# Optimization experiments

Measured on AMD Instinct MI355X. Metric: run time of the kernel, lower is better.

The kernel has to match this reference:

```python
import jax, jax.numpy as jnp
import numpy as np

BN_EPS = 1e-5

# Octonion multiplication table: hamilton block (r, c) = SIGN[c][r] * a[IDX[c][r]]
IDX = np.array([
    [0,1,2,3,4,5,6,7],
    [1,0,3,2,5,4,7,6],
    [2,3,0,1,6,7,4,5],
    [3,2,1,0,7,6,5,4],
    [4,5,6,7,0,1,2,3],
    [5,4,7,6,1,0,3,2],
    [6,7,4,5,2,3,0,1],
    [7,6,5,4,3,2,1,0]], dtype=np.int32)
SIGN = np.array([
    [ 1, 1, 1, 1, 1, 1, 1, 1],
    [ 1,-1, 1,-1, 1,-1,-1, 1],
    [ 1,-1,-1, 1, 1, 1,-1,-1],
    [ 1, 1,-1,-1, 1,-1, 1,-1],
    [ 1,-1,-1,-1,-1, 1, 1, 1],
    [ 1, 1,-1, 1,-1,-1,-1, 1],
    [ 1, 1, 1,-1,-1, 1,-1,-1],
    [ 1,-1, 1, 1,-1,-1, 1,-1]], dtype=np.float32)

def make_octonion_mul(kernel):
    # kernel: [in/8, out]; split cols into 8 chunks a0..a7 of [in/8, out/8]
    in8, out = kernel.shape
    out8 = out // 8
    a = kernel.reshape(in8, 8, out8).transpose(1, 0, 2)  # [8, in/8, out/8]
    blocks = jnp.asarray(SIGN)[:, :, None, None] * a[jnp.asarray(IDX)]  # [c, r, in/8, out/8]
    # hamilton[r*in8:(r+1)*in8, c*out8:(c+1)*out8] = blocks[c, r]
    return jnp.transpose(blocks, (1, 2, 0, 3)).reshape(8 * in8, out)  # [in, out]

def setup_inputs() -> dict:
    key = jax.random.key(0)
    ks = jax.random.split(key, 5)
    N, E, D_IN, D_OUT = 100000, 3200000, 256, 256
    stdv = float(np.sqrt(6.0 / (D_IN // 8 + D_OUT)))
    return {
        "x": jax.random.normal(ks[0], (N, D_IN), dtype=jnp.float32),
        "weight": jax.random.uniform(ks[1], (D_IN // 8, D_OUT), dtype=jnp.float32,
                                      minval=-stdv, maxval=stdv),
        "gamma": jnp.ones((D_OUT,), dtype=jnp.float32),
        "beta": jnp.zeros((D_OUT,), dtype=jnp.float32),
        "edge_weight": jax.random.uniform(ks[2], (E,), dtype=jnp.float32),
        "edge_src": jax.random.randint(ks[3], (E,), 0, N, dtype=jnp.int32),
        "edge_dst": jax.random.randint(ks[4], (E,), 0, N, dtype=jnp.int32),
    }

def reference(x, weight, gamma, beta, edge_weight, edge_src, edge_dst):
    N = x.shape[0]
    hamilton = make_octonion_mul(weight)          # [in, out]
    support = x @ hamilton                        # [N, out]
    # sparse adjacency aggregation: out[dst] += w * support[src]
    msgs = edge_weight[:, None] * support[edge_src]
    out = jax.ops.segment_sum(msgs, edge_dst, num_segments=N)  # [N, out]
    # BatchNorm1d (training mode: batch stats, biased variance)
    mean = jnp.mean(out, axis=0)
    var = jnp.var(out, axis=0)
    out = (out - mean) * jax.lax.rsqrt(var + BN_EPS) * gamma + beta
    return jnp.tanh(out)
```

## Files before the change

### kernel.cpp

```cpp
#include <hip/hip_runtime.h>
#include <cmath>

#define NB 512
#define CHUNK 8192

typedef short short8 __attribute__((ext_vector_type(8)));
typedef float f32x4 __attribute__((ext_vector_type(4)));

__constant__ int c_IDX[64] = {
  0,1,2,3,4,5,6,7,
  1,0,3,2,5,4,7,6,
  2,3,0,1,6,7,4,5,
  3,2,1,0,7,6,5,4,
  4,5,6,7,0,1,2,3,
  5,4,7,6,1,0,3,2,
  6,7,4,5,2,3,0,1,
  7,6,5,4,3,2,1,0};
__constant__ float c_SIGN[64] = {
  1,1,1,1,1,1,1,1,
  1,-1,1,-1,1,-1,-1,1,
  1,-1,-1,1,1,1,-1,-1,
  1,1,-1,-1,1,-1,1,-1,
  1,-1,-1,-1,-1,1,1,1,
  1,1,-1,1,-1,-1,-1,1,
  1,1,1,-1,-1,1,-1,-1,
  1,-1,1,1,-1,-1,1,-1};

__device__ inline unsigned bf16_rne(float f) {
  unsigned u = __float_as_uint(f);
  return (u + 0x7fffu + ((u >> 16) & 1u)) >> 16;
}
__device__ inline unsigned bfpack(float lo, float hi) {
  return bf16_rne(lo) | (bf16_rne(hi) << 16);
}

__global__ __launch_bounds__(256) void hamT_kernel(const float* __restrict__ weight,
                                                   unsigned short* __restrict__ hi,
                                                   unsigned short* __restrict__ lo) {
  int idx = blockIdx.x * 256 + threadIdx.x;
  int col = idx >> 8, k = idx & 255;
  int r = k >> 5, i = k & 31, c = col >> 5, o = col & 31;
  float v = c_SIGN[c * 8 + r] * weight[i * 256 + c_IDX[c * 8 + r] * 32 + o];
  unsigned hb = bf16_rne(v);
  float hf = __uint_as_float(hb << 16);
  hi[idx] = (unsigned short)hb;
  lo[idx] = (unsigned short)bf16_rne(v - hf);
}

__global__ __launch_bounds__(256) void cvt_kernel(const float4* __restrict__ x4,
                                                  uint2* __restrict__ xh, size_t n4) {
  size_t idx = (size_t)blockIdx.x * 256 + threadIdx.x;
  size_t stride = (size_t)gridDim.x * 256;
  for (size_t i = idx; i < n4; i += stride) {
    float4 v = x4[i];
    xh[i] = make_uint2(bfpack(v.x, v.y), bfpack(v.z, v.w));
  }
}

__global__ __launch_bounds__(256) void binhist_kernel(const int* __restrict__ dst,
                                                      int* __restrict__ binTot,
                                                      int E, int N) {
  __shared__ int h[NB];
  int tid = threadIdx.x;
  for (int i = tid; i < NB; i += 256) h[i] = 0;
  __syncthreads();
  int base = blockIdx.x * CHUNK;
  int end = base + CHUNK; if (end > E) end = E;
  for (int i = base + tid; i < end; i += 256)
    atomicAdd(&h[(int)((long long)dst[i] * NB / N)], 1);
  __syncthreads();
  for (int i = tid; i < NB; i += 256)
    if (h[i]) atomicAdd(&binTot[i], h[i]);
}

__global__ __launch_bounds__(512) void binscan_kernel(const int* __restrict__ binTot,
                                                      int* __restrict__ binStart,
                                                      int* __restrict__ binCursor, int E) {
  __shared__ int wsum[8], wbase[8];
  int tid = threadIdx.x, lane = tid & 63, wid = tid >> 6;
  int v = binTot[tid];
  int incl = v;
  #pragma unroll
  for (int d = 1; d < 64; d <<= 1) { int u = __shfl_up(incl, d); if (lane >= d) incl += u; }
  if (lane == 63) wsum[wid] = incl;
  __syncthreads();
  if (tid == 0) { int s = 0; for (int w = 0; w < 8; w++) { wbase[w] = s; s += wsum[w]; } }
  __syncthreads();
  int excl = wbase[wid] + incl - v;
  binStart[tid] = excl;
  binCursor[tid] = excl;
  if (tid == NB - 1) binStart[NB] = E;
}

__global__ __launch_bounds__(256) void bin_scatter(const int* __restrict__ src,
                                                   const int* __restrict__ dst,
                                                   const float* __restrict__ w,
                                                   int* __restrict__ binCursor,
                                                   int2* __restrict__ bb, int E, int N) {
  __shared__ int hist[NB];
  __shared__ int lcur[NB];
  int tid = threadIdx.x;
  int base = blockIdx.x * CHUNK;
  int end = base + CHUNK; if (end > E) end = E;
  for (int i = tid; i < NB; i += 256) hist[i] = 0;
  __syncthreads();
  for (int i = base + tid; i < end; i += 256)
    atomicAdd(&hist[(int)((long long)dst[i] * NB / N)], 1);
  __syncthreads();
  for (int i = tid; i < NB; i += 256) {
    int h = hist[i];
    lcur[i] = h ? atomicAdd(&binCursor[i], h) : 0;
  }
  __syncthreads();
  for (int i = base + tid; i < end; i += 256) {
    int d = dst[i];
    int b = (int)((long long)d * NB / N);
    int d0 = (int)(((long long)b * N + NB - 1) / NB);
    int pos = atomicAdd(&lcur[b], 1);
    bb[pos] = make_int2(src[i] | ((d - d0) << 24), __float_as_int(w[i]));
  }
}

__global__ __launch_bounds__(256) void bin_place(const int2* __restrict__ bb,
                                                 const int* __restrict__ binStart,
                                                 int* __restrict__ off,
                                                 int* __restrict__ cnt,
                                                 int2* __restrict__ edges, int N) {
  __shared__ int lcnt[208];
  __shared__ int loff[208];
  int b = blockIdx.x, tid = threadIdx.x;
  int d0 = (int)(((long long)b * N + NB - 1) / NB);
  int d1 = (int)(((long long)(b + 1) * N + NB - 1) / NB);
  if (d1 > N) d1 = N;
  int nd = d1 - d0;
  int e0 = binStart[b], e1 = binStart[b + 1];
  for (int i = tid; i < nd; i += 256) lcnt[i] = 0;
  __syncthreads();
  for (int i = e0 + tid; i < e1; i += 256)
    atomicAdd(&lcnt[((unsigned)bb[i].x) >> 24], 1);
  __syncthreads();
  if (tid == 0) {
    int s = e0;
    for (int i = 0; i < nd; i++) { loff[i] = s; s += lcnt[i]; }
  }
  __syncthreads();
  for (int i = tid; i < nd; i += 256) {
    off[d0 + i] = loff[i];
    cnt[d0 + i] = lcnt[i];
  }
  __syncthreads();
  for (int i = tid; i < nd; i += 256) lcnt[i] = loff[i];
  __syncthreads();
  for (int i = e0 + tid; i < e1; i += 256) {
    int2 e = bb[i];
    int pos = atomicAdd(&lcnt[((unsigned)e.x) >> 24], 1);
    edges[pos] = make_int2(e.x & 0xFFFFFF, e.y);
  }
}

__device__ inline void acc4(float& a0, float& a1, float& a2, float& a3,
                            uint2 v, float w) {
  a0 = fmaf(w, __uint_as_float(v.x << 16), a0);
  a1 = fmaf(w, __uint_as_float(v.x & 0xffff0000u), a1);
  a2 = fmaf(w, __uint_as_float(v.y << 16), a2);
  a3 = fmaf(w, __uint_as_float(v.y & 0xffff0000u), a3);
}

__global__ __launch_bounds__(256) void gather_kernel(const uint2* __restrict__ x8,
                                                     const int2* __restrict__ edges,
                                                     const int* __restrict__ off,
                                                     const int* __restrict__ cnt,
                                                     uint2* __restrict__ agg8, int N) {
  int d = blockIdx.x * 4 + (threadIdx.x >> 6);
  if (d >= N) return;
  int c = threadIdx.x & 63;
  int start = off[d], n = cnt[d];
  float a0 = 0.f, a1 = 0.f, a2 = 0.f, a3 = 0.f;
  int t = 0;
  for (; t + 8 <= n; t += 8) {
    int2 e0 = edges[start + t + 0];
    int2 e1 = edges[start + t + 1];
    int2 e2 = edges[start + t + 2];
    int2 e3 = edges[start + t + 3];
    int2 e4 = edges[start + t + 4];
    int2 e5 = edges[start + t + 5];
    int2 e6 = edges[start + t + 6];
    int2 e7 = edges[start + t + 7];
    uint2 v0 = x8[(size_t)e0.x * 64 + c];
    uint2 v1 = x8[(size_t)e1.x * 64 + c];
    uint2 v2 = x8[(size_t)e2.x * 64 + c];
    uint2 v3 = x8[(size_t)e3.x * 64 + c];
    uint2 v4 = x8[(size_t)e4.x * 64 + c];
    uint2 v5 = x8[(size_t)e5.x * 64 + c];
    uint2 v6 = x8[(size_t)e6.x * 64 + c];
    uint2 v7 = x8[(size_t)e7.x * 64 + c];
    acc4(a0, a1, a2, a3, v0, __int_as_float(e0.y));
    acc4(a0, a1, a2, a3, v1, __int_as_float(e1.y));
    acc4(a0, a1, a2, a3, v2, __int_as_float(e2.y));
    acc4(a0, a1, a2, a3, v3, __int_as_float(e3.y));
    acc4(a0, a1, a2, a3, v4, __int_as_float(e4.y));
    acc4(a0, a1, a2, a3, v5, __int_as_float(e5.y));
    acc4(a0, a1, a2, a3, v6, __int_as_float(e6.y));
    acc4(a0, a1, a2, a3, v7, __int_as_float(e7.y));
  }
  for (; t < n; t++) {
    int2 e0 = edges[start + t];
    uint2 v0 = x8[(size_t)e0.x * 64 + c];
    acc4(a0, a1, a2, a3, v0, __int_as_float(e0.y));
  }
  agg8[(size_t)d * 64 + c] = make_uint2(bfpack(a0, a1), bfpack(a2, a3));
}

__global__ __launch_bounds__(512) void mfma_gemm(const uint4* __restrict__ aggh,
                                                 const unsigned short* __restrict__ hamT_hi,
                                                 const unsigned short* __restrict__ hamT_lo,
                                                 float* __restrict__ bnsum,
                                                 float* __restrict__ out, int N) {
  __shared__ __align__(16) unsigned short Al[128 * 256];
  __shared__ float csum[256], csq[256];
  const int tid = threadIdx.x;
  const int row0 = blockIdx.x * 128;
  const int lane = tid & 63, wv = tid >> 6;
  const int wm = wv >> 2, wn = wv & 3;

  if (tid < 256) { csum[tid] = 0.f; csq[tid] = 0.f; }

  #pragma unroll
  for (int it = 0; it < 8; it++) {
    int cidx = it * 512 + tid;
    int row = cidx >> 5, c16 = cidx & 31;
    int rg = row0 + row;
    uint4 v = make_uint4(0u, 0u, 0u, 0u);
    if (rg < N) v = aggh[(size_t)rg * 32 + c16];
    *(uint4*)((char*)Al + row * 512 + ((c16 * 16) ^ ((row & 7) << 4))) = v;
  }
  __syncthreads();

  f32x4 acc[4][4];
  #pragma unroll
  for (int m = 0; m < 4; m++)
    #pragma unroll
    for (int n = 0; n < 4; n++) acc[m][n] = (f32x4)0.f;

  const char* bh = (const char*)hamT_hi;
  const char* bl = (const char*)hamT_lo;
  #pragma unroll
  for (int kk = 0; kk < 8; kk++) {
    const int kbyte = (lane >> 4) * 16 + kk * 64;
    short8 af[4];
    #pragma unroll
    for (int m = 0; m < 4; m++) {
      int row = wm * 64 + m * 16 + (lane & 15);
      af[m] = *(const short8*)((const char*)Al + row * 512 + (kbyte ^ ((row & 7) << 4)));
    }
    #pragma unroll
    for (int n = 0; n < 4; n++) {
      int colg = wn * 64 + n * 16 + (lane & 15);
      size_t boff = (size_t)colg * 512 + kbyte;
      short8 bhv = *(const short8*)(bh + boff);
      short8 blv = *(const short8*)(bl + boff);
      #pragma unroll
      for (int m = 0; m < 4; m++)
        acc[m][n] = __builtin_amdgcn_mfma_f32_16x16x32_bf16(af[m], bhv, acc[m][n], 0, 0, 0);
      #pragma unroll
      for (int m = 0; m < 4; m++)
        acc[m][n] = __builtin_amdgcn_mfma_f32_16x16x32_bf16(af[m], blv, acc[m][n], 0, 0, 0);
    }
  }

  #pragma unroll
  for (int n = 0; n < 4; n++) {
    int colg = wn * 64 + n * 16 + (lane & 15);
    float s = 0.f, q = 0.f;
    #pragma unroll
    for (int m = 0; m < 4; m++) {
      int rgb = row0 + wm * 64 + m * 16 + (lane >> 4) * 4;
      #pragma unroll
      for (int r = 0; r < 4; r++) {
        float v = acc[m][n][r];
        s += v; q = fmaf(v, v, q);
        int rg = rgb + r;
        if (rg < N) out[(size_t)rg * 256 + colg] = v;
      }
    }
    s += __shfl_xor(s, 16); s += __shfl_xor(s, 32);
    q += __shfl_xor(q, 16); q += __shfl_xor(q, 32);
    if (lane < 16) {
      atomicAdd(&csum[wn * 64 + n * 16 + lane], s);
      atomicAdd(&csq [wn * 64 + n * 16 + lane], q);
    }
  }
  __syncthreads();
  if (tid < 256) {
    atomicAdd(&bnsum[tid], csum[tid]);
    atomicAdd(&bnsum[256 + tid], csq[tid]);
  }
}

__global__ __launch_bounds__(256) void final_kernel(float* __restrict__ out,
                                                    const float* __restrict__ bnsum,
                                                    const float* __restrict__ gamma,
                                                    const float* __restrict__ beta,
                                                    float invN, size_t total4) {
  size_t idx = (size_t)blockIdx.x * 256 + threadIdx.x;
  size_t stride = (size_t)gridDim.x * 256;
  int c0 = (int)((idx * 4) & 255);
  float sc[4], ofs[4];
  #pragma unroll
  for (int j = 0; j < 4; j++) {
    float mean = bnsum[c0 + j] * invN;
    float var  = bnsum[256 + c0 + j] * invN - mean * mean;
    float s = rsqrtf(var + 1e-5f) * gamma[c0 + j];
    sc[j] = s;
    ofs[j] = beta[c0 + j] - mean * s;
  }
  float4* out4 = (float4*)out;
  for (size_t i = idx; i < total4; i += stride) {
    float4 v = out4[i];
    v.x = tanhf(fmaf(v.x, sc[0], ofs[0]));
    v.y = tanhf(fmaf(v.y, sc[1], ofs[1]));
    v.z = tanhf(fmaf(v.z, sc[2], ofs[2]));
    v.w = tanhf(fmaf(v.w, sc[3], ofs[3]));
    out4[i] = v;
  }
}

extern "C" void kernel_launch(void* const* d_in, const int* in_sizes, int n_in,
                              void* d_out, int out_size, void* d_ws, size_t ws_size,
                              hipStream_t stream) {
  const float* x      = (const float*)d_in[0];
  const float* weight = (const float*)d_in[1];
  const float* gamma  = (const float*)d_in[2];
  const float* beta   = (const float*)d_in[3];
  const float* ew     = (const float*)d_in[4];
  const int*   esrc   = (const int*)d_in[5];
  const int*   edst   = (const int*)d_in[6];
  const int N = in_sizes[0] / 256;
  const int E = in_sizes[4];
  float* out = (float*)d_out;

  char* p = (char*)d_ws;
  auto alloc = [&](size_t bytes) {
    char* q = p;
    p += (bytes + 255) & ~(size_t)255;
    return q;
  };
  unsigned short* hamT_hi = (unsigned short*)alloc(65536 * 2);
  unsigned short* hamT_lo = (unsigned short*)alloc(65536 * 2);
  int*   binTot    = (int*)alloc(NB * 4);
  int*   binStart  = (int*)alloc((NB + 1) * 4);
  int*   binCursor = (int*)alloc(NB * 4);
  int*   cnt       = (int*)alloc((size_t)N * 4);
  int*   off       = (int*)alloc((size_t)N * 4);
  int2*  bb        = (int2*)alloc((size_t)E * 8);
  int2*  edges     = (int2*)alloc((size_t)E * 8);
  uint2* xh        = (uint2*)alloc((size_t)N * 256 * 2);
  uint4* aggh      = (uint4*)alloc((size_t)N * 256 * 2);
  float* bnsum     = (float*)alloc(512 * 4);

  hipMemsetAsync(binTot, 0, NB * 4, stream);
  hipMemsetAsync(bnsum, 0, 512 * 4, stream);

  const int gridE = (E + CHUNK - 1) / CHUNK;
  const int rowBlocks = (N + 127) / 128;

  hamT_kernel<<<256, 256, 0, stream>>>(weight, hamT_hi, hamT_lo);
  cvt_kernel<<<2048, 256, 0, stream>>>((const float4*)x, xh, (size_t)N * 64);
  binhist_kernel<<<gridE, 256, 0, stream>>>(edst, binTot, E, N);
  binscan_kernel<<<1, 512, 0, stream>>>(binTot, binStart, binCursor, E);
  bin_scatter<<<gridE, 256, 0, stream>>>(esrc, edst, ew, binCursor, bb, E, N);
  bin_place<<<NB, 256, 0, stream>>>(bb, binStart, off, cnt, edges, N);
  gather_kernel<<<(N + 3) / 4, 256, 0, stream>>>((const uint2*)xh, edges, off, cnt,
                                                 (uint2*)aggh, N);
  mfma_gemm<<<rowBlocks, 512, 0, stream>>>(aggh, hamT_hi, hamT_lo, bnsum, out, N);
  final_kernel<<<2048, 256, 0, stream>>>(out, bnsum, gamma, beta, 1.f / (float)N,
                                         (size_t)N * 64);
}
```

Before: 501.7 us.

## Recompute GEMM in second pass to fuse BatchNorm and tanh into output write

```diff
diff --git a/kernel.cpp b/kernel.cpp
--- a/kernel.cpp
+++ b/kernel.cpp
@@ -215,7 +215,11 @@
                                                  const unsigned short* __restrict__ hamT_hi,
                                                  const unsigned short* __restrict__ hamT_lo,
                                                  float* __restrict__ bnsum,
-                                                 float* __restrict__ out, int N) {
+                                                 const float* __restrict__ gamma,
+                                                 const float* __restrict__ beta,
+                                                 float invN,
+                                                 float* __restrict__ out,
+                                                 int N, int phase) {
   __shared__ __align__(16) unsigned short Al[128 * 256];
   __shared__ float csum[256], csq[256];
   const int tid = threadIdx.x;
@@ -223,7 +227,7 @@
   const int lane = tid & 63, wv = tid >> 6;
   const int wm = wv >> 2, wn = wv & 3;
 
-  if (tid < 256) { csum[tid] = 0.f; csq[tid] = 0.f; }
+  if (phase == 0 && tid < 256) { csum[tid] = 0.f; csq[tid] = 0.f; }
 
   #pragma unroll
   for (int it = 0; it < 8; it++) {
@@ -268,60 +272,44 @@
     }
   }
 
-  #pragma unroll
-  for (int n = 0; n < 4; n++) {
-    int colg = wn * 64 + n * 16 + (lane & 15);
-    float s = 0.f, q = 0.f;
-    #pragma unroll
-    for (int m = 0; m < 4; m++) {
-      int rgb = row0 + wm * 64 + m * 16 + (lane >> 4) * 4;
+  if (phase == 0) {
+    #pragma unroll
+    for (int n = 0; n < 4; n++) {
+      float s = 0.f, q = 0.f;
       #pragma unroll
-      for (int r = 0; r < 4; r++) {
-        float v = acc[m][n][r];
-        s += v; q = fmaf(v, v, q);
-        int rg = rgb + r;
-        if (rg < N) out[(size_t)rg * 256 + colg] = v;
+      for (int m = 0; m < 4; m++)
+        #pragma unroll
+        for (int r = 0; r < 4; r++) { float v = acc[m][n][r]; s += v; q = fmaf(v, v, q); }
+      s += __shfl_xor(s, 16); s += __shfl_xor(s, 32);
+      q += __shfl_xor(q, 16); q += __shfl_xor(q, 32);
+      if (lane < 16) {
+        atomicAdd(&csum[wn * 64 + n * 16 + lane], s);
+        atomicAdd(&csq [wn * 64 + n * 16 + lane], q);
       }
     }
-    s += __shfl_xor(s, 16); s += __shfl_xor(s, 32);
-    q += __shfl_xor(q, 16); q += __shfl_xor(q, 32);
-    if (lane < 16) {
-      atomicAdd(&csum[wn * 64 + n * 16 + lane], s);
-      atomicAdd(&csq [wn * 64 + n * 16 + lane], q);
-    }
-  }
-  __syncthreads();
-  if (tid < 256) {
-    atomicAdd(&bnsum[tid], csum[tid]);
-    atomicAdd(&bnsum[256 + tid], csq[tid]);
-  }
-}
-
-__global__ __launch_bounds__(256) void final_kernel(float* __restrict__ out,
-                                                    const float* __restrict__ bnsum,
-                                                    const float* __restrict__ gamma,
-                                                    const float* __restrict__ beta,
-                                                    float invN, size_t total4) {
-  size_t idx = (size_t)blockIdx.x * 256 + threadIdx.x;
-  size_t stride = (size_t)gridDim.x * 256;
-  int c0 = (int)((idx * 4) & 255);
-  float sc[4], ofs[4];
-  #pragma unroll
-  for (int j = 0; j < 4; j++) {
-    float mean = bnsum[c0 + j] * invN;
-    float var  = bnsum[256 + c0 + j] * invN - mean * mean;
-    float s = rsqrtf(var + 1e-5f) * gamma[c0 + j];
-    sc[j] = s;
-    ofs[j] = beta[c0 + j] - mean * s;
-  }
-  float4* out4 = (float4*)out;
-  for (size_t i = idx; i < total4; i += stride) {
-    float4 v = out4[i];
-    v.x = tanhf(fmaf(v.x, sc[0], ofs[0]));
-    v.y = tanhf(fmaf(v.y, sc[1], ofs[1]));
-    v.z = tanhf(fmaf(v.z, sc[2], ofs[2]));
-    v.w = tanhf(fmaf(v.w, sc[3], ofs[3]));
-    out4[i] = v;
+    __syncthreads();
+    if (tid < 256) {
+      atomicAdd(&bnsum[tid], csum[tid]);
+      atomicAdd(&bnsum[256 + tid], csq[tid]);
+    }
+  } else {
+    #pragma unroll
+    for (int n = 0; n < 4; n++) {
+      int colg = wn * 64 + n * 16 + (lane & 15);
+      float mean = bnsum[colg] * invN;
+      float var  = bnsum[256 + colg] * invN - mean * mean;
+      float sc = rsqrtf(var + 1e-5f) * gamma[colg];
+      float ofs = beta[colg] - mean * sc;
+      #pragma unroll
+      for (int m = 0; m < 4; m++) {
+        int rgb = row0 + wm * 64 + m * 16 + (lane >> 4) * 4;
+        #pragma unroll
+        for (int r = 0; r < 4; r++) {
+          int rg = rgb + r;
+          if (rg < N) out[(size_t)rg * 256 + colg] = tanhf(fmaf(acc[m][n][r], sc, ofs));
+        }
+      }
+    }
   }
 }
 
@@ -363,6 +351,7 @@
 
   const int gridE = (E + CHUNK - 1) / CHUNK;
   const int rowBlocks = (N + 127) / 128;
+  const float invN = 1.f / (float)N;
 
   hamT_kernel<<<256, 256, 0, stream>>>(weight, hamT_hi, hamT_lo);
   cvt_kernel<<<2048, 256, 0, stream>>>((const float4*)x, xh, (size_t)N * 64);
@@ -372,7 +361,8 @@
   bin_place<<<NB, 256, 0, stream>>>(bb, binStart, off, cnt, edges, N);
   gather_kernel<<<(N + 3) / 4, 256, 0, stream>>>((const uint2*)xh, edges, off, cnt,
                                                  (uint2*)aggh, N);
-  mfma_gemm<<<rowBlocks, 512, 0, stream>>>(aggh, hamT_hi, hamT_lo, bnsum, out, N);
-  final_kernel<<<2048, 256, 0, stream>>>(out, bnsum, gamma, beta, 1.f / (float)N,
-                                         (size_t)N * 64);
-}
+  mfma_gemm<<<rowBlocks, 512, 0, stream>>>(aggh, hamT_hi, hamT_lo, bnsum,
+                                           gamma, beta, invN, out, N, 0);
+  mfma_gemm<<<rowBlocks, 512, 0, stream>>>(aggh, hamT_hi, hamT_lo, bnsum,
+                                           gamma, beta, invN, out, N, 1);
+}
```

After: 558.2 us. 1.11x slower.
